# Optimization experiments

Measured on AMD Instinct MI355X. Metric: run time of the kernel, lower is better.

Reference implementation:

```python
import jax, jax.numpy as jnp
import numpy as np
from functools import partial

CONF_THRESH = 0.01
NMS_THRESH = 0.45
TOP_K = 200


def setup_inputs() -> dict:
    key = jax.random.key(0)
    k1, k2, k3 = jax.random.split(key, 3)
    B, N, C = 256, 8732, 21
    loc_data = jax.random.normal(k1, (B, N, 4), dtype=jnp.float32)
    conf_data = jax.random.normal(k2, (B, N, C), dtype=jnp.float32)
    dbox_list = jax.random.uniform(k3, (N, 4), dtype=jnp.float32)
    return {"loc_data": loc_data, "conf_data": conf_data, "dbox_list": dbox_list}


def decode(loc, dbox):
    # loc, dbox: (N, 4). Faithful to torch decode: variances 0.1 / 0.2.
    cxcy = dbox[:, :2] + loc[:, :2] * 0.1 * dbox[:, 2:]
    wh = dbox[:, 2:] * jnp.exp(loc[:, 2:] * 0.2)
    xymin = cxcy - wh / 2.0
    xymax = xymin + wh
    return jnp.concatenate([xymin, xymax], axis=1)  # (N,4) xmin,ymin,xmax,ymax


def nms_single(boxes, scores):
    # boxes: (N,4), scores: (N,). Returns (TOP_K, 5) rows [conf, x1, y1, x2, y2]
    # compacted to the front in descending-score keep order (matches torch output[i,cl,:count]).
    masked = jnp.where(scores > CONF_THRESH, scores, -1.0)
    top_scores, top_idx = jax.lax.top_k(masked, TOP_K)
    b = boxes[top_idx]  # (TOP_K, 4)
    x1, y1, x2, y2 = b[:, 0], b[:, 1], b[:, 2], b[:, 3]
    area = (x2 - x1) * (y2 - y1)
    valid = top_scores > CONF_THRESH

    def body(i, state):
        suppressed, keep = state
        active = jnp.logical_not(suppressed[i])
        keep = keep.at[i].set(active)
        # Faithful to source: all four coords are clamped with min=coord[i]
        # (i.e. elementwise max), including x2/y2 -- reproducing the original math.
        xx1 = jnp.maximum(x1, x1[i])
        yy1 = jnp.maximum(y1, y1[i])
        xx2 = jnp.maximum(x2, x2[i])
        yy2 = jnp.maximum(y2, y2[i])
        inter = (xx2 - xx1) * (yy2 - yy1)
        union = area - inter + area[i]
        iou = inter / union
        sup_new = jnp.logical_and(active, iou > NMS_THRESH)
        sup_new = sup_new.at[i].set(False)
        return jnp.logical_or(suppressed, sup_new), keep

    suppressed0 = jnp.logical_not(valid)
    keep0 = jnp.zeros((TOP_K,), dtype=bool)
    suppressed, keep = jax.lax.fori_loop(0, TOP_K, body, (suppressed0, keep0))

    rows = jnp.concatenate([top_scores[:, None], b], axis=1)  # (TOP_K, 5)
    rows = jnp.where(keep[:, None], rows, 0.0)
    dest = jnp.where(keep, jnp.cumsum(keep) - 1, TOP_K)  # dump slot TOP_K
    out = jnp.zeros((TOP_K + 1, 5), dtype=boxes.dtype).at[dest].set(rows)
    return out[:TOP_K]


def reference(loc_data, conf_data, dbox_list):
    # loc_data: (B, 8732, 4); conf_data: (B, 8732, 21); dbox_list: (8732, 4)
    conf = jax.nn.softmax(conf_data, axis=-1)          # (B, N, C)
    conf_preds = jnp.transpose(conf, (0, 2, 1))        # (B, C, N)
    decoded = jax.vmap(decode, in_axes=(0, None))(loc_data, dbox_list)  # (B, N, 4)
    per_class = jax.vmap(lambda bx, sc: jax.vmap(lambda s: nms_single(bx, s))(sc))(
        decoded, conf_preds
    )  # (B, C, TOP_K, 5)
    # class 0 is background and is skipped in the torch loop -> zeros
    return per_class.at[:, 0].set(0.0)
```

## Files before the change

kernel.cpp:

```cpp
#include <hip/hip_runtime.h>
#include <cstdint>

#pragma clang fp contract(off)

#define TPB 256
typedef unsigned int uint32;
typedef unsigned short u16;
typedef unsigned long long u64;

constexpr int BB = 256;
constexpr int NN = 8732;
constexpr int CC = 21;
constexpr int KK = 200;
constexpr int CH = (NN + TPB - 1) / TPB;
constexpr uint32 KBIAS = 0x3C23D70Au;

__device__ __forceinline__ double fexp(double a) {
  const double L2E = 1.4426950408889634074;
  const double SHIFT = 6755399441055744.0;
  double t = __builtin_fma(a, L2E, SHIFT);
  int i = (int)__double_as_longlong(t);
  double n = t - SHIFT;
  double r = __builtin_fma(n, -6.93147180369123816490e-01, a);
  r = __builtin_fma(n, -1.90821492927058770002e-10, r);
  double p = 1.6059043836821614599e-10;
  p = __builtin_fma(p, r, 2.0876756987868098979e-9);
  p = __builtin_fma(p, r, 2.5052108385441718775e-8);
  p = __builtin_fma(p, r, 2.7557319223985890653e-7);
  p = __builtin_fma(p, r, 2.7557319223985890653e-6);
  p = __builtin_fma(p, r, 2.4801587301587301587e-5);
  p = __builtin_fma(p, r, 1.9841269841269841270e-4);
  p = __builtin_fma(p, r, 1.3888888888888888889e-3);
  p = __builtin_fma(p, r, 8.3333333333333333333e-3);
  p = __builtin_fma(p, r, 4.1666666666666666667e-2);
  p = __builtin_fma(p, r, 1.6666666666666666667e-1);
  p = __builtin_fma(p, r, 0.5);
  p = __builtin_fma(p, r, 1.0);
  p = __builtin_fma(p, r, 1.0);
  return p * __longlong_as_double((long long)(1023 + i) << 52);
}

__device__ __forceinline__ float exp_f32_exact(float xf) {
  double v = fexp((double)xf);
  uint32 low29 = (uint32)__double_as_longlong(v) & 0x1FFFFFFFu;
  uint32 dist = (low29 > 0x10000000u) ? (low29 - 0x10000000u) : (0x10000000u - low29);
  if (__builtin_expect(dist <= 65536u, 0)) v = exp((double)xf);
  return (float)v;
}

__device__ __forceinline__ u64 rfl64(u64 v) {
  uint32 lo = (uint32)__builtin_amdgcn_readfirstlane((int)(uint32)v);
  uint32 hi = (uint32)__builtin_amdgcn_readfirstlane((int)(uint32)(v >> 32));
  return ((u64)hi << 32) | lo;
}

struct NmsS {
  alignas(16) float bx1[256];
  alignas(16) float by1[256];
  alignas(16) float bx2[256];
  alignas(16) float by2[256];
  alignas(16) float barea[256];
  alignas(16) float bscore[256];
  alignas(16) u64 mask[KK][4];
  u64 kept[4];
};
struct SmemT {
  union alignas(16) UU {
    u16 s16[NN];
    NmsS nms;
  } u;
  union alignas(16) HC {
    uint32 hist[512];
    u64 cand[256];
  } hc;
  uint32 sc4[4];
  uint32 bc[3];
  uint32 slot;
};
static_assert(sizeof(SmemT) <= 20 * 1024, "LDS budget for 8 blocks/CU");

__device__ __forceinline__ uint32 kk_of(float p) {
  return (p > 0.01f) ? (__float_as_uint(p) - KBIAS) : 0u;
}

__device__ __forceinline__ void scan_find(SmemT& sm, uint32 target, int t, int lane, int wv,
                                          uint32& pivot, uint32& cntabove, uint32& pivcnt,
                                          uint32& total) {
  uint32 h0 = sm.hc.hist[2 * t], h1 = sm.hc.hist[2 * t + 1];
  uint32 part = h0 + h1;
  uint32 suf = part;
  for (int off = 1; off < 64; off <<= 1) {
    uint32 v = __shfl_down(suf, off, 64);
    if (lane + off < 64) suf += v;
  }
  if (lane == 0) sm.sc4[wv] = suf;
  __syncthreads();
  uint32 tot = sm.sc4[0] + sm.sc4[1] + sm.sc4[2] + sm.sc4[3];
  uint32 add = 0;
  for (int w = wv + 1; w < 4; ++w) add += sm.sc4[w];
  uint32 mine = suf + add, nxt = mine - part;
  if (mine >= target && nxt < target) {
    uint32 acc = nxt + h1;
    if (acc >= target) { sm.bc[0] = 2u * t + 1u; sm.bc[1] = nxt; sm.bc[2] = h1; }
    else               { sm.bc[0] = 2u * t;      sm.bc[1] = acc; sm.bc[2] = h0; }
  }
  __syncthreads();
  sm.hc.hist[2 * t] = 0u;
  sm.hc.hist[2 * t + 1] = 0u;
  pivot = sm.bc[0];
  cntabove = sm.bc[1];
  pivcnt = sm.bc[2];
  total = tot;
  __syncthreads();
}

template <int MODE>
__global__ __launch_bounds__(TPB, 5) void prep_kernel(const float* __restrict__ conf,
                                                      float* __restrict__ probsT,
                                                      double2* __restrict__ ms) {
  __shared__ float tile[TPB * CC];
  const int blk = blockIdx.x;
  const int b = blockIdx.y;
  const int n0 = blk * TPB;
  const int cnt = (NN - n0 < TPB) ? (NN - n0) : TPB;
  const size_t base = ((size_t)b * NN + n0) * CC;
  if (cnt == TPB) {
    const float4* s4 = (const float4*)(conf + base);
    float4* t4 = (float4*)tile;
    for (int i = threadIdx.x; i < (TPB * CC) / 4; i += TPB) t4[i] = s4[i];
  } else {
    for (int i = threadIdx.x; i < cnt * CC; i += TPB) tile[i] = conf[base + i];
  }
  __syncthreads();
  if (threadIdx.x >= cnt) return;
  const int n = n0 + threadIdx.x;
  const float* cp = tile + threadIdx.x * CC;
  float mx = cp[0];
#pragma unroll
  for (int j = 1; j < CC; ++j) mx = fmaxf(mx, cp[j]);
  const double mxd = (double)mx;

  if (MODE == 0) {
    double es1[CC - 1];
    double S = fexp((double)cp[0] - mxd);
#pragma unroll
    for (int j = 1; j < CC; ++j) {
      es1[j - 1] = fexp((double)cp[j] - mxd);
      S += es1[j - 1];
    }
    const double Sinv = 1.0 / S;
    bool slow = false;
    float* op = probsT + (size_t)b * 20 * NN + n;
#pragma unroll
    for (int c2 = 1; c2 < CC; ++c2) {
      double ph = es1[c2 - 1] * Sinv;
      uint32 low29 = (uint32)__double_as_longlong(ph) & 0x1FFFFFFFu;
      uint32 dist = (low29 > 0x10000000u) ? (low29 - 0x10000000u) : (0x10000000u - low29);
      slow = slow || (dist <= 320u) || (ph < 1e-30);
      op[(size_t)(c2 - 1) * NN] = (float)ph;
    }
    if (__builtin_expect(slow, 0)) {
      double es2[CC];
      double S2 = 0.0;
      for (int j = 0; j < CC; ++j) {
        es2[j] = exp((double)cp[j] - mxd);
        S2 += es2[j];
      }
      double Si2 = 1.0 / S2;
      for (int c2 = 1; c2 < CC; ++c2) op[(size_t)(c2 - 1) * NN] = (float)(es2[c2] * Si2);
    }
  } else {
    double S = 0.0;
#pragma unroll
    for (int j = 0; j < CC; ++j) S += exp((double)cp[j] - mxd);
    ms[(size_t)b * NN + n] = make_double2(mxd, 1.0 / S);
  }
}

template <int MODE>
__device__ __forceinline__ float prob_one(const float* __restrict__ prow,
                                          const float* __restrict__ conf,
                                          const double2* __restrict__ ms,
                                          int b, int c, int n) {
  if (MODE == 0) {
    return prow[n];
  } else if (MODE == 1) {
    double2 mv = ms[(size_t)b * NN + n];
    float x = conf[((size_t)b * NN + n) * CC + c];
    return (float)(exp((double)x - mv.x) * mv.y);
  } else {
    const float* cp = conf + ((size_t)b * NN + n) * CC;
    float mx = cp[0];
    for (int j = 1; j < CC; ++j) mx = fmaxf(mx, cp[j]);
    double S = 0.0, ec = 0.0;
    for (int j = 0; j < CC; ++j) {
      double e = exp((double)cp[j] - (double)mx);
      S += e;
      if (j == c) ec = e;
    }
    return (float)(ec * (1.0 / S));
  }
}

__device__ __forceinline__ void mask_unit32(NmsS& nm, int r, int c) {
  const double MD = 0x1.CCCCCDp-2;
  const float xi1 = nm.bx1[r], yi1 = nm.by1[r];
  const float xi2 = nm.bx2[r], yi2 = nm.by2[r];
  const float ai = nm.barea[r];
  const int jbeg = c * 32;
  uint32 w = 0;
#pragma unroll
  for (int j0 = jbeg; j0 < jbeg + 32; j0 += 4) {
    const float4 q1 = *(const float4*)&nm.bx1[j0];
    const float4 q2 = *(const float4*)&nm.by1[j0];
    const float4 q3 = *(const float4*)&nm.bx2[j0];
    const float4 q4 = *(const float4*)&nm.by2[j0];
    const float4 qa = *(const float4*)&nm.barea[j0];
    const float a1[4] = {q1.x, q1.y, q1.z, q1.w};
    const float a2[4] = {q2.x, q2.y, q2.z, q2.w};
    const float a3[4] = {q3.x, q3.y, q3.z, q3.w};
    const float a4[4] = {q4.x, q4.y, q4.z, q4.w};
    const float aa[4] = {qa.x, qa.y, qa.z, qa.w};
#pragma unroll
    for (int e = 0; e < 4; ++e) {
      const int j = j0 + e;
      float xx1 = fmaxf(a1[e], xi1);
      float yy1 = fmaxf(a2[e], yi1);
      float xx2 = fmaxf(a3[e], xi2);
      float yy2 = fmaxf(a4[e], yi2);
      float inter = (xx2 - xx1) * (yy2 - yy1);
      float uni = (aa[e] - inter) + ai;
      bool sup = (uni >= 0.0f) && ((double)inter > MD * (double)uni);
      if (sup) w |= 1u << (j & 31);
    }
  }
  const int d = r - jbeg;
  if (d >= 0) w &= (0xFFFFFFFEu << d);
  ((uint32*)&nm.mask[r][0])[c] = w;
}

__device__ __forceinline__ void mask_unit_short(NmsS& nm, int r) {
  const double MD = 0x1.CCCCCDp-2;
  const float xi1 = nm.bx1[r], yi1 = nm.by1[r];
  const float xi2 = nm.bx2[r], yi2 = nm.by2[r];
  const float ai = nm.barea[r];
  uint32 w = 0;
#pragma unroll
  for (int j0 = 192; j0 < 200; j0 += 4) {
    const float4 q1 = *(const float4*)&nm.bx1[j0];
    const float4 q2 = *(const float4*)&nm.by1[j0];
    const float4 q3 = *(const float4*)&nm.bx2[j0];
    const float4 q4 = *(const float4*)&nm.by2[j0];
    const float4 qa = *(const float4*)&nm.barea[j0];
    const float a1[4] = {q1.x, q1.y, q1.z, q1.w};
    const float a2[4] = {q2.x, q2.y, q2.z, q2.w};
    const float a3[4] = {q3.x, q3.y, q3.z, q3.w};
    const float a4[4] = {q4.x, q4.y, q4.z, q4.w};
    const float aa[4] = {qa.x, qa.y, qa.z, qa.w};
#pragma unroll
    for (int e = 0; e < 4; ++e) {
      const int j = j0 + e;
      float xx1 = fmaxf(a1[e], xi1);
      float yy1 = fmaxf(a2[e], yi1);
      float xx2 = fmaxf(a3[e], xi2);
      float yy2 = fmaxf(a4[e], yi2);
      float inter = (xx2 - xx1) * (yy2 - yy1);
      float uni = (aa[e] - inter) + ai;
      bool sup = (uni >= 0.0f) && ((double)inter > MD * (double)uni);
      if (sup) w |= 1u << (j & 31);
    }
  }
  const int d = r - 192;
  if (d >= 0) w &= (0xFFFFFFFEu << d);
  ((uint32*)&nm.mask[r][0])[6] = w;
}

template <int MODE>
__global__ __launch_bounds__(TPB, 8) void nms_kernel(
    const float* __restrict__ probsT, const float* __restrict__ conf,
    const double2* __restrict__ ms, const float* __restrict__ loc,
    const float* __restrict__ dbox, float* __restrict__ out) {
  __shared__ SmemT sm;
  const int t = threadIdx.x;
  const int lane = t & 63;
  const int wv = t >> 6;
  const int tb = blockIdx.x;
  const int xcd = tb & 7;
  const int s0i = tb >> 3;
  const int bi = s0i / CC;
  const int c = s0i - bi * CC;
  const int b = bi * 8 + xcd;
  const size_t outbase = (size_t)(b * CC + c) * KK * 5;

  if (c == 0) {
    for (int i = t; i < KK * 5; i += TPB) out[outbase + i] = 0.0f;
    return;
  }
  const float* prow = (MODE == 0) ? probsT + ((size_t)b * 20 + (c - 1)) * NN : nullptr;

  sm.hc.hist[t] = 0u;
  sm.hc.hist[t + 256] = 0u;
  if (t == 0) sm.slot = 0u;
  __syncthreads();

  if (MODE == 0) {
    const float4* p4 = (const float4*)prow;
    for (int i = t; i < NN / 4; i += TPB) {
      float4 p = p4[i];
      uint32 k0 = kk_of(p.x), k1 = kk_of(p.y), k2 = kk_of(p.z), k3 = kk_of(p.w);
      uint32 s0 = k0 ? (k0 >> 10) + 1u : 0u;
      uint32 s1 = k1 ? (k1 >> 10) + 1u : 0u;
      uint32 s2 = k2 ? (k2 >> 10) + 1u : 0u;
      uint32 s3 = k3 ? (k3 >> 10) + 1u : 0u;
      ((u64*)sm.u.s16)[i] = (u64)s0 | ((u64)s1 << 16) | ((u64)s2 << 32) | ((u64)s3 << 48);
      if (s0) atomicAdd(&sm.hc.hist[s0 >> 8], 1u);
      if (s1) atomicAdd(&sm.hc.hist[s1 >> 8], 1u);
      if (s2) atomicAdd(&sm.hc.hist[s2 >> 8], 1u);
      if (s3) atomicAdd(&sm.hc.hist[s3 >> 8], 1u);
    }
  } else {
    for (int n = t; n < NN; n += TPB) {
      uint32 k = kk_of(prob_one<MODE>(prow, conf, ms, b, c, n));
      uint32 s = k ? (k >> 10) + 1u : 0u;
      sm.u.s16[n] = (u16)s;
      if (s) atomicAdd(&sm.hc.hist[s >> 8], 1u);
    }
  }
  __syncthreads();
  uint32 P0, cg0, pc0, total;
  scan_find(sm, (uint32)KK, t, lane, wv, P0, cg0, pc0, total);

  const bool few = total < (uint32)KK;
  uint32 P16, cgA = 0, eqc = 0, ncand;
  if (!few) {
    for (int i = t; i < NN / 2; i += TPB) {
      uint32 w = ((const uint32*)sm.u.s16)[i];
      uint32 a = w & 0xFFFFu, bq = w >> 16;
      if ((a >> 8) == P0) atomicAdd(&sm.hc.hist[a & 0xFFu], 1u);
      if ((bq >> 8) == P0) atomicAdd(&sm.hc.hist[bq & 0xFFu], 1u);
    }
    __syncthreads();
    uint32 P1, cg1, pc1, tot1;
    scan_find(sm, (uint32)KK - cg0, t, lane, wv, P1, cg1, pc1, tot1);
    P16 = (P0 << 8) | P1;
    cgA = cg0 + cg1;
    eqc = pc1;
    ncand = cgA + eqc;
  } else {
    P16 = 1u;
    ncand = total;
  }

  u64 val = 0;
  if (ncand <= 256u) {
    sm.hc.cand[t] = 0ull;
    __syncthreads();
    for (int i = t; i < NN / 2; i += TPB) {
      uint32 w = ((const uint32*)sm.u.s16)[i];
      uint32 a = w & 0xFFFFu, bq = w >> 16;
      if (a >= P16) { uint32 s = atomicAdd(&sm.slot, 1u); sm.hc.cand[s] = (u64)(2 * i); }
      if (bq >= P16) { uint32 s = atomicAdd(&sm.slot, 1u); sm.hc.cand[s] = (u64)(2 * i + 1); }
    }
    __syncthreads();
    if (few) {
      const int base = t * CH;
      const int endn = (base + CH < NN) ? (base + CH) : NN;
      uint32 cz = 0;
      for (int n = base; n < endn; ++n) cz += (sm.u.s16[n] == 0);
      uint32 incl = cz;
      for (int off = 1; off < 64; off <<= 1) {
        uint32 v = __shfl_up(incl, off, 64);
        if (lane >= off) incl += v;
      }
      if (lane == 63) sm.sc4[wv] = incl;
      __syncthreads();
      uint32 add = 0;
      for (int w2 = 0; w2 < wv; ++w2) add += sm.sc4[w2];
      uint32 g = add + incl - cz;
      const uint32 npad = (uint32)KK - ncand;
      if (cz && g < npad) {
        for (int n = base; n < endn && g < npad; ++n)
          if (sm.u.s16[n] == 0) { sm.hc.cand[ncand + g] = (u64)n; ++g; }
      }
      __syncthreads();
    }
    const uint32 ntot = few ? (uint32)KK : ncand;
    if (t < (int)ntot) {
      uint32 idx = (uint32)sm.hc.cand[t];
      uint32 k = (t < (int)ncand) ? kk_of(prob_one<MODE>(prow, conf, ms, b, c, (int)idx)) : 0u;
      val = ((u64)k << 32) | (uint32)(~idx);
    }
  } else {
    const uint32 BK = P16 - 1u;
    const uint32 tgt = (uint32)KK - cgA;
    for (int n = t; n < NN; n += TPB) {
      uint32 k = kk_of(prob_one<MODE>(prow, conf, ms, b, c, n));
      if (k && (k >> 10) == BK) atomicAdd(&sm.hc.hist[(k >> 5) & 31u], 1u);
    }
    __syncthreads();
    uint32 q0, d0, px, tx;
    scan_find(sm, tgt, t, lane, wv, q0, d0, px, tx);
    for (int n = t; n < NN; n += TPB) {
      uint32 k = kk_of(prob_one<MODE>(prow, conf, ms, b, c, n));
      if (k && (k >> 5) == ((BK << 5) | q0)) atomicAdd(&sm.hc.hist[k & 31u], 1u);
    }
    __syncthreads();
    uint32 q1, d1, py, ty;
    scan_find(sm, tgt - d0, t, lane, wv, q1, d1, py, ty);
    const uint32 T = (BK << 10) | (q0 << 5) | q1;
    const uint32 cnt_gt = cgA + d0 + d1;
    const uint32 m_need = (uint32)KK - cnt_gt;
    sm.hc.cand[t] = 0ull;
    if (t == 0) sm.slot = 0u;
    __syncthreads();
    const int base = t * CH;
    const int endn = (base + CH < NN) ? (base + CH) : NN;
    uint32 cnteq = 0;
    for (int n = base; n < endn; ++n) {
      uint32 k = kk_of(prob_one<MODE>(prow, conf, ms, b, c, n));
      if (k > T) {
        uint32 s = atomicAdd(&sm.slot, 1u);
        sm.hc.cand[s] = ((u64)k << 32) | (uint32)(~(uint32)n);
      }
      cnteq += (k == T);
    }
    uint32 incl = cnteq;
    for (int off = 1; off < 64; off <<= 1) {
      uint32 v = __shfl_up(incl, off, 64);
      if (lane >= off) incl += v;
    }
    if (lane == 63) sm.sc4[wv] = incl;
    __syncthreads();
    uint32 add = 0;
    for (int w2 = 0; w2 < wv; ++w2) add += sm.sc4[w2];
    uint32 g = add + incl - cnteq;
    if (cnteq && g < m_need) {
      for (int n = base; n < endn && g < m_need; ++n) {
        uint32 k = kk_of(prob_one<MODE>(prow, conf, ms, b, c, n));
        if (k == T) {
          sm.hc.cand[cnt_gt + g] = ((u64)T << 32) | (uint32)(~(uint32)n);
          ++g;
        }
      }
    }
    __syncthreads();
    val = sm.hc.cand[t];
  }

  for (int kk = 2; kk <= 256; kk <<= 1) {
    for (int j = kk >> 1; j > 0; j >>= 1) {
      u64 other;
      if (j >= 64) {
        __syncthreads();
        sm.hc.cand[t] = val;
        __syncthreads();
        other = sm.hc.cand[t ^ j];
      } else {
        other = __shfl_xor((unsigned long long)val, j, 64);
      }
      const bool takeMax = ((t & kk) == 0) == ((t & j) == 0);
      val = takeMax ? (val > other ? val : other) : (val < other ? val : other);
    }
  }
  __syncthreads();

  if (t < KK) {
    uint32 k32 = (uint32)(val >> 32);
    uint32 idx = ~((uint32)val);
    bool valid = k32 != 0u;
    float score = valid ? __uint_as_float(k32 + KBIAS) : -1.0f;
    const float4 lc = ((const float4*)loc)[(size_t)b * NN + idx];
    const float4 db = ((const float4*)dbox)[idx];
    float cx = db.x + (lc.x * 0.1f) * db.z;
    float cy = db.y + (lc.y * 0.1f) * db.w;
    float w_ = db.z * exp_f32_exact(lc.z * 0.2f);
    float h_ = db.w * exp_f32_exact(lc.w * 0.2f);
    float x1 = cx - w_ * 0.5f;
    float y1 = cy - h_ * 0.5f;
    float x2 = x1 + w_;
    float y2 = y1 + h_;
    sm.u.nms.bx1[t] = x1;
    sm.u.nms.by1[t] = y1;
    sm.u.nms.bx2[t] = x2;
    sm.u.nms.by2[t] = y2;
    sm.u.nms.barea[t] = (x2 - x1) * (y2 - y1);
    sm.u.nms.bscore[t] = score;
  } else {
    sm.u.nms.bscore[t] = -1.0f;
  }
  __syncthreads();

  {
    {
      int u = t;
      int cq = (u >= 192) ? ((u >= 480) ? 5 : ((u >= 320) ? 4 : 3))
                          : ((u >= 96) ? 2 : ((u >= 32) ? 1 : 0));
      int off = 16 * cq * (cq + 1);
      mask_unit32(sm.u.nms, u - off, cq);
    }
    {
      int u = 256 + t;
      int cq = (u >= 480) ? 5 : ((u >= 320) ? 4 : 3);
      int off = 16 * cq * (cq + 1);
      mask_unit32(sm.u.nms, u - off, cq);
    }
    if (t < 160) {
      int u = 512 + t;
      mask_unit32(sm.u.nms, u - 480, 5);
    }
    if (t < KK) mask_unit_short(sm.u.nms, t);
  }
  __syncthreads();

  if (wv == 0) {
    u64 s0 = __ballot(!(sm.u.nms.bscore[lane] > 0.01f));
    u64 s1 = __ballot(!(sm.u.nms.bscore[64 + lane] > 0.01f));
    u64 s2 = __ballot(!(sm.u.nms.bscore[128 + lane] > 0.01f));
    u64 s3 = __ballot(!(sm.u.nms.bscore[192 + lane] > 0.01f)) | ~0xFFull;
    u64 k0 = 0, k1 = 0, k2 = 0, k3 = 0;
    const u64(*M)[4] = sm.u.nms.mask;
    u64 pre[4][4];
#pragma unroll
    for (int s = 0; s < 4; ++s) {
      ulonglong2 a = ((const ulonglong2*)M[s])[0];
      ulonglong2 bb = ((const ulonglong2*)M[s])[1];
      pre[s][0] = a.x; pre[s][1] = a.y; pre[s][2] = bb.x; pre[s][3] = bb.y;
    }
#define WALK_BLOCK(SW, KW, CNT, IBASE)                                   \
  _Pragma("unroll 4")                                                    \
  for (int ii = 0; ii < (CNT); ++ii) {                                   \
    const int s = ii & 3;                                                \
    u64 c0 = rfl64(pre[s][0]), c1 = rfl64(pre[s][1]);                    \
    u64 c2 = rfl64(pre[s][2]), c3 = rfl64(pre[s][3]);                    \
    const int inext = (IBASE) + ii + 4;                                  \
    ulonglong2 na = ((const ulonglong2*)M[inext])[0];                    \
    ulonglong2 nb = ((const ulonglong2*)M[inext])[1];                    \
    pre[s][0] = na.x; pre[s][1] = na.y; pre[s][2] = nb.x; pre[s][3] = nb.y; \
    u64 bm = 1ull << ii;                                                 \
    if (!((SW) & bm)) {                                                  \
      (KW) |= bm;                                                        \
      s0 |= c0; s1 |= c1; s2 |= c2; s3 |= c3;                            \
    }                                                                    \
  }
    WALK_BLOCK(s0, k0, 64, 0)
    WALK_BLOCK(s1, k1, 64, 64)
    WALK_BLOCK(s2, k2, 64, 128)
    WALK_BLOCK(s3, k3, 8, 192)
#undef WALK_BLOCK
    if (lane == 0) {
      sm.u.nms.kept[0] = k0; sm.u.nms.kept[1] = k1;
      sm.u.nms.kept[2] = k2; sm.u.nms.kept[3] = k3;
    }
  } else {
    float4 z4 = make_float4(0.f, 0.f, 0.f, 0.f);
    float4* o4 = (float4*)(out + outbase);
    for (int i = t - 64; i < (KK * 5) / 4; i += 192) o4[i] = z4;
  }
  __syncthreads();

  if (t < KK) {
    const u64 K0 = sm.u.nms.kept[0], K1 = sm.u.nms.kept[1];
    const u64 K2 = sm.u.nms.kept[2], K3 = sm.u.nms.kept[3];
    const int w = t >> 6;
    const int bit = t & 63;
    u64 kw = (w == 0) ? K0 : (w == 1) ? K1 : (w == 2) ? K2 : K3;
    bool kp = (kw >> bit) & 1ull;
    if (kp) {
      u64 lowm = (bit == 0) ? 0ull : (~0ull >> (64 - bit));
      int d = __popcll(kw & lowm);
      if (w > 0) d += __popcll(K0);
      if (w > 1) d += __popcll(K1);
      if (w > 2) d += __popcll(K2);
      float* o = out + outbase + (size_t)d * 5;
      o[0] = sm.u.nms.bscore[t];
      o[1] = sm.u.nms.bx1[t];
      o[2] = sm.u.nms.by1[t];
      o[3] = sm.u.nms.bx2[t];
      o[4] = sm.u.nms.by2[t];
    }
  }
}

extern "C" void kernel_launch(void* const* d_in, const int* in_sizes, int n_in,
                              void* d_out, int out_size, void* d_ws, size_t ws_size,
                              hipStream_t stream) {
  (void)in_sizes; (void)n_in; (void)out_size;
  const float* loc = (const float*)d_in[0];
  const float* conf = (const float*)d_in[1];
  const float* dbox = (const float*)d_in[2];
  float* out = (float*)d_out;

  const size_t needA = (size_t)BB * 20 * NN * sizeof(float);
  const size_t needB = (size_t)BB * NN * sizeof(double2);
  dim3 blk(TPB);
  dim3 g1((NN + TPB - 1) / TPB, BB);
  const int g2 = BB * CC;

  if (ws_size >= needA) {
    float* probsT = (float*)d_ws;
    prep_kernel<0><<<g1, blk, 0, stream>>>(conf, probsT, nullptr);
    nms_kernel<0><<<g2, blk, 0, stream>>>(probsT, conf, nullptr, loc, dbox, out);
  } else if (ws_size >= needB) {
    double2* msp = (double2*)d_ws;
    prep_kernel<1><<<g1, blk, 0, stream>>>(conf, nullptr, msp);
    nms_kernel<1><<<g2, blk, 0, stream>>>(nullptr, conf, msp, loc, dbox, out);
  } else {
    nms_kernel<2><<<g2, blk, 0, stream>>>(nullptr, conf, nullptr, loc, dbox, out);
  }
}
```

Measured before the change: 468.3 us.

## Transpose NMS suppression mask to per-lane columns and walk with ballots

Stores the suppression mask transposed, so each box has a 9-word padded column of bits recording which earlier boxes suppress it, and rebalances the mask work units over the triangle. The serial keep walk in wave 0 changes from scalar readfirstlane broadcasts of 256-bit rows plus a prefetch ring to per-lane suppression flags that are updated from register-held mask words and re-ballotted only when a box is kept. This is meant to remove the per-step LDS row loads and scalar broadcasts from the critical serial loop. In exchange it adds a ballot per kept box, the mask must be zeroed first, and the fully unrolled loops may raise register use and code size.

```diff
diff --git a/kernel.cpp b/kernel.cpp
--- a/kernel.cpp
+++ b/kernel.cpp
@@ -48,12 +48,6 @@
   return (float)v;
 }
 
-__device__ __forceinline__ u64 rfl64(u64 v) {
-  uint32 lo = (uint32)__builtin_amdgcn_readfirstlane((int)(uint32)v);
-  uint32 hi = (uint32)__builtin_amdgcn_readfirstlane((int)(uint32)(v >> 32));
-  return ((u64)hi << 32) | lo;
-}
-
 struct NmsS {
   alignas(16) float bx1[256];
   alignas(16) float by1[256];
@@ -61,7 +55,7 @@
   alignas(16) float by2[256];
   alignas(16) float barea[256];
   alignas(16) float bscore[256];
-  alignas(16) u64 mask[KK][4];
+  alignas(16) uint32 maskT[256 * 9];
   u64 kept[4];
 };
 struct SmemT {
@@ -202,20 +196,20 @@
   }
 }
 
-__device__ __forceinline__ void mask_unit32(NmsS& nm, int r, int c) {
+__device__ __forceinline__ void mask_unitT(NmsS& nm, int c, int k) {
   const double MD = 0x1.CCCCCDp-2;
-  const float xi1 = nm.bx1[r], yi1 = nm.by1[r];
-  const float xi2 = nm.bx2[r], yi2 = nm.by2[r];
-  const float ai = nm.barea[r];
-  const int jbeg = c * 32;
+  const float xi1 = nm.bx1[c], yi1 = nm.by1[c];
+  const float xi2 = nm.bx2[c], yi2 = nm.by2[c];
+  const float ai = nm.barea[c];
+  const int rbeg = k * 32;
   uint32 w = 0;
 #pragma unroll
-  for (int j0 = jbeg; j0 < jbeg + 32; j0 += 4) {
-    const float4 q1 = *(const float4*)&nm.bx1[j0];
-    const float4 q2 = *(const float4*)&nm.by1[j0];
-    const float4 q3 = *(const float4*)&nm.bx2[j0];
-    const float4 q4 = *(const float4*)&nm.by2[j0];
-    const float4 qa = *(const float4*)&nm.barea[j0];
+  for (int r0 = rbeg; r0 < rbeg + 32; r0 += 4) {
+    const float4 q1 = *(const float4*)&nm.bx1[r0];
+    const float4 q2 = *(const float4*)&nm.by1[r0];
+    const float4 q3 = *(const float4*)&nm.bx2[r0];
+    const float4 q4 = *(const float4*)&nm.by2[r0];
+    const float4 qa = *(const float4*)&nm.barea[r0];
     const float a1[4] = {q1.x, q1.y, q1.z, q1.w};
     const float a2[4] = {q2.x, q2.y, q2.z, q2.w};
     const float a3[4] = {q3.x, q3.y, q3.z, q3.w};
@@ -223,7 +217,7 @@
     const float aa[4] = {qa.x, qa.y, qa.z, qa.w};
 #pragma unroll
     for (int e = 0; e < 4; ++e) {
-      const int j = j0 + e;
+      const int r = r0 + e;
       float xx1 = fmaxf(a1[e], xi1);
       float yy1 = fmaxf(a2[e], yi1);
       float xx2 = fmaxf(a3[e], xi2);
@@ -231,48 +225,12 @@
       float inter = (xx2 - xx1) * (yy2 - yy1);
       float uni = (aa[e] - inter) + ai;
       bool sup = (uni >= 0.0f) && ((double)inter > MD * (double)uni);
-      if (sup) w |= 1u << (j & 31);
-    }
-  }
-  const int d = r - jbeg;
-  if (d >= 0) w &= (0xFFFFFFFEu << d);
-  ((uint32*)&nm.mask[r][0])[c] = w;
-}
-
-__device__ __forceinline__ void mask_unit_short(NmsS& nm, int r) {
-  const double MD = 0x1.CCCCCDp-2;
-  const float xi1 = nm.bx1[r], yi1 = nm.by1[r];
-  const float xi2 = nm.bx2[r], yi2 = nm.by2[r];
-  const float ai = nm.barea[r];
-  uint32 w = 0;
-#pragma unroll
-  for (int j0 = 192; j0 < 200; j0 += 4) {
-    const float4 q1 = *(const float4*)&nm.bx1[j0];
-    const float4 q2 = *(const float4*)&nm.by1[j0];
-    const float4 q3 = *(const float4*)&nm.bx2[j0];
-    const float4 q4 = *(const float4*)&nm.by2[j0];
-    const float4 qa = *(const float4*)&nm.barea[j0];
-    const float a1[4] = {q1.x, q1.y, q1.z, q1.w};
-    const float a2[4] = {q2.x, q2.y, q2.z, q2.w};
-    const float a3[4] = {q3.x, q3.y, q3.z, q3.w};
-    const float a4[4] = {q4.x, q4.y, q4.z, q4.w};
-    const float aa[4] = {qa.x, qa.y, qa.z, qa.w};
-#pragma unroll
-    for (int e = 0; e < 4; ++e) {
-      const int j = j0 + e;
-      float xx1 = fmaxf(a1[e], xi1);
-      float yy1 = fmaxf(a2[e], yi1);
-      float xx2 = fmaxf(a3[e], xi2);
-      float yy2 = fmaxf(a4[e], yi2);
-      float inter = (xx2 - xx1) * (yy2 - yy1);
-      float uni = (aa[e] - inter) + ai;
-      bool sup = (uni >= 0.0f) && ((double)inter > MD * (double)uni);
-      if (sup) w |= 1u << (j & 31);
-    }
-  }
-  const int d = r - 192;
-  if (d >= 0) w &= (0xFFFFFFFEu << d);
-  ((uint32*)&nm.mask[r][0])[6] = w;
+      if (sup) w |= 1u << (r & 31);
+    }
+  }
+  const int d = c - rbeg;
+  if (d < 32) w &= (1u << d) - 1u;
+  nm.maskT[c * 9 + k] = w;
 }
 
 template <int MODE>
@@ -464,6 +422,11 @@
   }
   __syncthreads();
 
+  {
+    uint32* mz = sm.u.nms.maskT + t * 9;
+#pragma unroll
+    for (int q = 0; q < 9; ++q) mz[q] = 0u;
+  }
   if (t < KK) {
     uint32 k32 = (uint32)(val >> 32);
     uint32 idx = ~((uint32)val);
@@ -491,65 +454,61 @@
   __syncthreads();
 
   {
-    {
-      int u = t;
-      int cq = (u >= 192) ? ((u >= 480) ? 5 : ((u >= 320) ? 4 : 3))
-                          : ((u >= 96) ? 2 : ((u >= 32) ? 1 : 0));
-      int off = 16 * cq * (cq + 1);
-      mask_unit32(sm.u.nms, u - off, cq);
-    }
-    {
-      int u = 256 + t;
-      int cq = (u >= 480) ? 5 : ((u >= 320) ? 4 : 3);
-      int off = 16 * cq * (cq + 1);
-      mask_unit32(sm.u.nms, u - off, cq);
-    }
-    if (t < 160) {
-      int u = 512 + t;
-      mask_unit32(sm.u.nms, u - 480, 5);
-    }
-    if (t < KK) mask_unit_short(sm.u.nms, t);
+    auto do_unit = [&](int u) {
+      int cq, k;
+      if (u < 199)      { k = 0; cq = u + 1; }
+      else if (u < 366) { k = 1; cq = u - 166; }
+      else if (u < 501) { k = 2; cq = u - 301; }
+      else if (u < 604) { k = 3; cq = u - 404; }
+      else if (u < 675) { k = 4; cq = u - 475; }
+      else if (u < 714) { k = 5; cq = u - 514; }
+      else              { k = 6; cq = u - 521; }
+      mask_unitT(sm.u.nms, cq, k);
+    };
+    do_unit(t);
+    do_unit(256 + t);
+    if (t >= 47) do_unit(512 + (255 - t));
   }
   __syncthreads();
 
   if (wv == 0) {
-    u64 s0 = __ballot(!(sm.u.nms.bscore[lane] > 0.01f));
-    u64 s1 = __ballot(!(sm.u.nms.bscore[64 + lane] > 0.01f));
-    u64 s2 = __ballot(!(sm.u.nms.bscore[128 + lane] > 0.01f));
-    u64 s3 = __ballot(!(sm.u.nms.bscore[192 + lane] > 0.01f)) | ~0xFFull;
-    u64 k0 = 0, k1 = 0, k2 = 0, k3 = 0;
-    const u64(*M)[4] = sm.u.nms.mask;
-    u64 pre[4][4];
-#pragma unroll
-    for (int s = 0; s < 4; ++s) {
-      ulonglong2 a = ((const ulonglong2*)M[s])[0];
-      ulonglong2 bb = ((const ulonglong2*)M[s])[1];
-      pre[s][0] = a.x; pre[s][1] = a.y; pre[s][2] = bb.x; pre[s][3] = bb.y;
-    }
-#define WALK_BLOCK(SW, KW, CNT, IBASE)                                   \
-  _Pragma("unroll 4")                                                    \
-  for (int ii = 0; ii < (CNT); ++ii) {                                   \
-    const int s = ii & 3;                                                \
-    u64 c0 = rfl64(pre[s][0]), c1 = rfl64(pre[s][1]);                    \
-    u64 c2 = rfl64(pre[s][2]), c3 = rfl64(pre[s][3]);                    \
-    const int inext = (IBASE) + ii + 4;                                  \
-    ulonglong2 na = ((const ulonglong2*)M[inext])[0];                    \
-    ulonglong2 nb = ((const ulonglong2*)M[inext])[1];                    \
-    pre[s][0] = na.x; pre[s][1] = na.y; pre[s][2] = nb.x; pre[s][3] = nb.y; \
-    u64 bm = 1ull << ii;                                                 \
-    if (!((SW) & bm)) {                                                  \
-      (KW) |= bm;                                                        \
-      s0 |= c0; s1 |= c1; s2 |= c2; s3 |= c3;                            \
-    }                                                                    \
-  }
-    WALK_BLOCK(s0, k0, 64, 0)
-    WALK_BLOCK(s1, k1, 64, 64)
-    WALK_BLOCK(s2, k2, 64, 128)
-    WALK_BLOCK(s3, k3, 8, 192)
-#undef WALK_BLOCK
+    uint32 sf0 = (sm.u.nms.bscore[lane] > 0.01f) ? 0u : 1u;
+    uint32 sf1 = (sm.u.nms.bscore[64 + lane] > 0.01f) ? 0u : 1u;
+    uint32 sf2 = (sm.u.nms.bscore[128 + lane] > 0.01f) ? 0u : 1u;
+    uint32 sf3 = (lane >= 8) ? 1u : ((sm.u.nms.bscore[192 + lane] > 0.01f) ? 0u : 1u);
+    const uint32* MT = sm.u.nms.maskT;
+    const int l0 = lane * 9, l1 = (64 + lane) * 9, l2 = (128 + lane) * 9, l3 = (192 + lane) * 9;
+    u64 kept0, kept1, kept2, kept3;
+
+#define WBLK(W, CNT, KOUT, SF)                                                 \
+  {                                                                            \
+    uint32 a0 = MT[l0 + 2 * W], b0 = MT[l0 + 2 * W + 1];                       \
+    uint32 a1 = MT[l1 + 2 * W], b1 = MT[l1 + 2 * W + 1];                       \
+    uint32 a2 = MT[l2 + 2 * W], b2 = MT[l2 + 2 * W + 1];                       \
+    uint32 a3 = MT[l3 + 2 * W], b3 = MT[l3 + 2 * W + 1];                       \
+    u64 S = __ballot(SF != 0u);                                                \
+    u64 kw = 0;                                                                \
+    _Pragma("unroll")                                                          \
+    for (int ii = 0; ii < (CNT); ++ii) {                                       \
+      if (!((S >> ii) & 1ull)) {                                               \
+        kw |= 1ull << ii;                                                      \
+        sf0 |= (ii < 32) ? ((a0 >> ii) & 1u) : ((b0 >> (ii - 32)) & 1u);       \
+        sf1 |= (ii < 32) ? ((a1 >> ii) & 1u) : ((b1 >> (ii - 32)) & 1u);       \
+        sf2 |= (ii < 32) ? ((a2 >> ii) & 1u) : ((b2 >> (ii - 32)) & 1u);       \
+        sf3 |= (ii < 32) ? ((a3 >> ii) & 1u) : ((b3 >> (ii - 32)) & 1u);       \
+        S = __ballot(SF != 0u);                                                \
+      }                                                                        \
+    }                                                                          \
+    KOUT = kw;                                                                 \
+  }
+    WBLK(0, 64, kept0, sf0)
+    WBLK(1, 64, kept1, sf1)
+    WBLK(2, 64, kept2, sf2)
+    WBLK(3, 8, kept3, sf3)
+#undef WBLK
     if (lane == 0) {
-      sm.u.nms.kept[0] = k0; sm.u.nms.kept[1] = k1;
-      sm.u.nms.kept[2] = k2; sm.u.nms.kept[3] = k3;
+      sm.u.nms.kept[0] = kept0; sm.u.nms.kept[1] = kept1;
+      sm.u.nms.kept[2] = kept2; sm.u.nms.kept[3] = kept3;
     }
   } else {
     float4 z4 = make_float4(0.f, 0.f, 0.f, 0.f);
```

Result: slower. 551.2 us (+17.7%).
